# Performance work log

Measured on AMD Instinct MI355X. Metric: run time of the kernel, lower is better.

## Reference

```python
import jax, jax.numpy as jnp
import numpy as np

HID, AA, ESM = 128, 21, 320
D1 = HID + AA + ESM          # 469
N_GRAPHS = 64
BN_EPS = 1e-5


def _lin_params(key, din, dout):
    k1, k2 = jax.random.split(key)
    s = 1.0 / np.sqrt(din)
    W = jax.random.uniform(k1, (din, dout), jnp.float32, -s, s)
    b = jax.random.uniform(k2, (dout,), jnp.float32, -s, s)
    return W, b


def setup_inputs() -> dict:
    key = jax.random.key(0)
    ks = jax.random.split(key, 16)
    N, E = 30000, 480000
    inp = {
        'prot_x': jax.random.normal(ks[0], (N, 6485), jnp.float32),
        'prot_edge_index': jax.random.randint(ks[1], (2, E), 0, N, jnp.int64),
        'prot_batch': jnp.sort(jax.random.randint(ks[2], (N,), 0, N_GRAPHS, jnp.int64)),
    }
    inp['fl1_W'], inp['fl1_b'] = _lin_params(ks[3], 6165 - 21, HID)
    inp['fl2_W'], inp['fl2_b'] = _lin_params(ks[4], AA, AA)
    inp['fl3_W'], inp['fl3_b'] = _lin_params(ks[5], ESM, ESM)
    inp['pdb1_W'], inp['pdb1_b'] = _lin_params(ks[6], D1, D1)
    inp['pdb2_W'], inp['pdb2_b'] = _lin_params(ks[7], D1, 2 * D1)
    inp['af1_W'], inp['af1_b'] = _lin_params(ks[8], D1, D1)
    inp['af2_W'], inp['af2_b'] = _lin_params(ks[9], D1, 2 * D1)
    inp['pdb3_W'], inp['pdb3_b'] = _lin_params(ks[10], 4 * D1, 4 * D1)
    inp['fc1_W'], inp['fc1_b'] = _lin_params(ks[11], 4 * D1, 1024)
    inp['bn_g'] = jnp.ones((1024,), jnp.float32)
    inp['bn_b'] = jnp.zeros((1024,), jnp.float32)
    inp['fc2_W'], inp['fc2_b'] = _lin_params(ks[12], 1024, 486)
    return inp


def _gcn_graph(edge_index, n):
    # add self-loops, symmetric normalization D^-1/2 (A+I) D^-1/2
    loops = jnp.arange(n, dtype=edge_index.dtype)
    src = jnp.concatenate([edge_index[0], loops])
    dst = jnp.concatenate([edge_index[1], loops])
    deg = jax.ops.segment_sum(jnp.ones_like(dst, jnp.float32), dst, n)
    dinv = jax.lax.rsqrt(jnp.maximum(deg, 1.0))  # deg >= 1 via self-loop
    norm = dinv[src] * dinv[dst]
    return src, dst, norm


def _gcn_conv(x, W, b, src, dst, norm, n):
    h = x @ W                                   # [N, Dout]
    msg = h[src] * norm[:, None]                # gather + scale
    return jax.ops.segment_sum(msg, dst, n) + b  # scatter-add


def reference(prot_x, prot_edge_index, prot_batch,
              fl1_W, fl1_b, fl2_W, fl2_b, fl3_W, fl3_b,
              pdb1_W, pdb1_b, pdb2_W, pdb2_b,
              af1_W, af1_b, af2_W, af2_b,
              pdb3_W, pdb3_b, fc1_W, fc1_b, bn_g, bn_b, fc2_W, fc2_b):
    n = prot_x.shape[0]
    relu = jax.nn.relu
    f1 = relu(prot_x[:, 21:6165] @ fl1_W + fl1_b)   # [N,128]
    f2 = relu(prot_x[:, :21] @ fl2_W + fl2_b)       # [N,21]
    f3 = relu(prot_x[:, 6165:] @ fl3_W + fl3_b)     # [N,320]
    feat = jnp.concatenate([f2, f1, f3], axis=1)    # [N,469]

    src, dst, norm = _gcn_graph(prot_edge_index, n)
    x = relu(_gcn_conv(feat, pdb1_W, pdb1_b, src, dst, norm, n))
    x = relu(_gcn_conv(x, pdb2_W, pdb2_b, src, dst, norm, n))
    y = relu(_gcn_conv(feat, af1_W, af1_b, src, dst, norm, n))
    y = relu(_gcn_conv(y, af2_W, af2_b, src, dst, norm, n))
    z = jnp.concatenate([x, y], axis=1)             # [N, 4*469]
    z = relu(_gcn_conv(z, pdb3_W, pdb3_b, src, dst, norm, n))

    # gap: global mean pool per graph
    cnt = jax.ops.segment_sum(jnp.ones((n,), jnp.float32), prot_batch, N_GRAPHS)
    z = jax.ops.segment_sum(z, prot_batch, N_GRAPHS) / jnp.maximum(cnt, 1.0)[:, None]

    z = z @ fc1_W + fc1_b                            # [G,1024]
    mu = jnp.mean(z, axis=0)
    var = jnp.mean((z - mu) ** 2, axis=0)            # biased, torch BN training math
    z = (z - mu) * jax.lax.rsqrt(var + BN_EPS) * bn_g + bn_b
    z = relu(z)                                      # dropout = identity (eval)
    z = z @ fc2_W + fc2_b
    return jax.nn.sigmoid(z)
```

## Files before the change

### kernel.cpp

```cpp
#include <hip/hip_runtime.h>
#include <hip/hip_bf16.h>
#include <stdint.h>

#define NG 64

typedef __attribute__((ext_vector_type(8))) short bf16x8;
typedef __attribute__((ext_vector_type(4))) float f32x4;

#define AS1 __attribute__((address_space(1)))
#define AS3 __attribute__((address_space(3)))

static __device__ __forceinline__ unsigned short f2b(float f) {
    unsigned u = __float_as_uint(f);
    return (unsigned short)((u + 0x7fffu + ((u >> 16) & 1u)) >> 16);
}
static __device__ __forceinline__ float b2f(unsigned short h) {
    return __uint_as_float(((unsigned)h) << 16);
}
static __device__ __forceinline__ void gl16(const void* g, void* l) {
    __builtin_amdgcn_global_load_lds(
        (const AS1 void*)(uintptr_t)g,
        (AS3 void*)(unsigned)(uintptr_t)l, 16, 0, 0);
}

__global__ void initcnt_k(int* cnt, int n) {
    int i = blockIdx.x * blockDim.x + threadIdx.x;
    if (i < n) cnt[i] = 0;
}
__global__ void count_k(const int* __restrict__ dst, int* cnt, int E) {
    int e = blockIdx.x * blockDim.x + threadIdx.x;
    if (e < E) atomicAdd(&cnt[dst[e]], 1);
}
__global__ void dinv_k(const int* __restrict__ cnt, float* dinv, int n) {
    int i = blockIdx.x * blockDim.x + threadIdx.x;
    if (i < n) dinv[i] = rsqrtf((float)(cnt[i] + 1));
}
__global__ void exscan_k(const int* __restrict__ cnt, int* rowptr, int n) {
    __shared__ int wsum[16];
    __shared__ int carry;
    int tid = threadIdx.x, lane = tid & 63, wid = tid >> 6;
    if (tid == 0) { carry = 0; rowptr[0] = 0; }
    __syncthreads();
    for (int base = 0; base < n; base += 1024) {
        int i = base + tid;
        int x = (i < n) ? cnt[i] : 0;
#pragma unroll
        for (int off = 1; off < 64; off <<= 1) {
            int t = __shfl_up(x, off);
            if (lane >= off) x += t;
        }
        if (lane == 63) wsum[wid] = x;
        __syncthreads();
        if (tid < 16) {
            int s = wsum[tid];
#pragma unroll
            for (int off = 1; off < 16; off <<= 1) {
                int t = __shfl_up(s, off);
                if (tid >= off) s += t;
            }
            wsum[tid] = s;
        }
        __syncthreads();
        int add = carry + (wid ? wsum[wid - 1] : 0);
        if (i < n) rowptr[i + 1] = x + add;
        __syncthreads();
        if (tid == 1023) carry = x + add;
        __syncthreads();
    }
}
__global__ void fillinit_k(const int* __restrict__ rowptr, int* fill, int n) {
    int i = blockIdx.x * blockDim.x + threadIdx.x;
    if (i < n) fill[i] = rowptr[i];
}
__global__ void fill_k(const int* __restrict__ src, const int* __restrict__ dst,
                       int* fill, int* csr, int E) {
    int e = blockIdx.x * blockDim.x + threadIdx.x;
    if (e < E) {
        int d = dst[e];
        int pos = atomicAdd(&fill[d], 1);
        csr[pos] = src[e];
    }
}

__global__ void wtconv_k(const float* __restrict__ W, int K, int Nout,
                         unsigned short* __restrict__ Wt, int Kpad) {
    __shared__ float t[32][33];
    int k0 = blockIdx.x * 32, n0 = blockIdx.y * 32;
    int cx = threadIdx.x & 31, ry = threadIdx.x >> 5;
#pragma unroll
    for (int p = 0; p < 4; ++p) {
        int k = k0 + ry + p * 8, nn = n0 + cx;
        t[ry + p * 8][cx] = (k < K && nn < Nout) ? W[(size_t)k * Nout + nn] : 0.0f;
    }
    __syncthreads();
#pragma unroll
    for (int p = 0; p < 4; ++p) {
        int nn = n0 + ry + p * 8, k = k0 + cx;
        Wt[(size_t)nn * Kpad + k] = f2b(t[cx][ry + p * 8]);
    }
}

__global__ void fl2_k(const float* __restrict__ x, int ldx,
                      const float* __restrict__ W, const float* __restrict__ b,
                      unsigned short* __restrict__ out, int ldo, int n) {
    __shared__ float Ws[441];
    __shared__ float Bs[21];
    int tid = threadIdx.x;
    for (int i = tid; i < 441; i += 256) Ws[i] = W[i];
    if (tid < 21) Bs[tid] = b[tid];
    __syncthreads();
    int row = blockIdx.x * 256 + tid;
    if (row >= n) return;
    float xv[21];
#pragma unroll
    for (int j = 0; j < 21; ++j) xv[j] = x[(size_t)row * ldx + j];
    for (int c = 0; c < 21; ++c) {
        float a = Bs[c];
#pragma unroll
        for (int j = 0; j < 21; ++j) a = fmaf(xv[j], Ws[j * 21 + c], a);
        out[(size_t)row * ldo + c] = f2b(fmaxf(a, 0.0f));
    }
}

template<int BNT, bool A32>
__global__ __launch_bounds__(256) void mgemm_t(
    const void* __restrict__ Aptr, int lda, int Mreal,
    const unsigned short* __restrict__ Bt, int ldb,
    const float* __restrict__ bias,
    unsigned short* __restrict__ C, int ldc, int coff,
    int K, int Nout, int Nzero, int GX) {
    constexpr int NI = BNT / 32;
    __shared__ unsigned short As[128 * 32];
    __shared__ unsigned short Bs[BNT * 32];
    const int tid = threadIdx.x;
    const int w = tid >> 6, lane = tid & 63;

    const int nwg = gridDim.x;
    const int q = nwg >> 3, r = nwg & 7;
    const int xcd = blockIdx.x & 7, oidx = blockIdx.x >> 3;
    const int swz = (xcd < r ? xcd * (q + 1) : r * (q + 1) + (xcd - r) * q) + oidx;
    const int m0 = (swz / GX) * 128, n0 = (swz % GX) * BNT;

    const int wr = w >> 1, wc = w & 1;

    f32x4 acc[4][NI];
#pragma unroll
    for (int i = 0; i < 4; ++i)
#pragma unroll
        for (int j = 0; j < NI; ++j) acc[i][j] = (f32x4){0.f, 0.f, 0.f, 0.f};

    const int ko = (lane >> 4) * 8;
    const int rA = wr * 64 + (lane & 15);
    const int rB = wc * (BNT / 2) + (lane & 15);

    for (int k0 = 0; k0 < K; k0 += 32) {
        if constexpr (A32) {
            const float* Af = (const float*)Aptr;
#pragma unroll
            for (int j = 0; j < 2; ++j) {
                int c = w * 2 + j;
                int id2 = c * 64 + lane;
                int row = id2 >> 2, cc = id2 & 3;
                int gm = m0 + row; if (gm > Mreal - 1) gm = Mreal - 1;
                const float* ap = Af + (size_t)gm * lda + k0 + cc * 8;
                float4 v0 = *(const float4*)ap;
                float4 v1 = *(const float4*)(ap + 4);
                unsigned short t[8] = {f2b(v0.x), f2b(v0.y), f2b(v0.z), f2b(v0.w),
                                       f2b(v1.x), f2b(v1.y), f2b(v1.z), f2b(v1.w)};
                *(bf16x8*)&As[row * 32 + cc * 8] = *(const bf16x8*)t;
            }
        } else {
            const unsigned short* Ab = (const unsigned short*)Aptr;
#pragma unroll
            for (int j = 0; j < 2; ++j) {
                int c = w * 2 + j;
                int id2 = c * 64 + lane;
                int row = id2 >> 2, cc = id2 & 3;
                gl16(Ab + (size_t)(m0 + row) * lda + k0 + cc * 8, &As[c * 512]);
            }
        }
#pragma unroll
        for (int j = 0; j < BNT / 64; ++j) {
            int c = w * (BNT / 64) + j;
            int id2 = c * 64 + lane;
            int row = id2 >> 2, cc = id2 & 3;
            gl16(Bt + (size_t)(n0 + row) * ldb + k0 + cc * 8, &Bs[c * 512]);
        }
        __syncthreads();
        bf16x8 a[4], b[NI];
#pragma unroll
        for (int i = 0; i < 4; ++i) a[i] = *(const bf16x8*)&As[(rA + i * 16) * 32 + ko];
#pragma unroll
        for (int j = 0; j < NI; ++j) b[j] = *(const bf16x8*)&Bs[(rB + j * 16) * 32 + ko];
#pragma unroll
        for (int i = 0; i < 4; ++i)
#pragma unroll
            for (int j = 0; j < NI; ++j)
                acc[i][j] = __builtin_amdgcn_mfma_f32_16x16x32_bf16(a[i], b[j], acc[i][j], 0, 0, 0);
        __syncthreads();
    }

    const int cn = lane & 15, r4 = (lane >> 4) * 4;
    for (int ni = 0; ni < NI; ++ni) {
        int col = n0 + wc * (BNT / 2) + ni * 16 + cn;
        if (col >= Nzero) continue;
        bool real = col < Nout;
        float bb = real ? bias[col] : 0.0f;
#pragma unroll
        for (int mi = 0; mi < 4; ++mi) {
#pragma unroll
            for (int rr = 0; rr < 4; ++rr) {
                int row = m0 + wr * 64 + mi * 16 + r4 + rr;
                float x = real ? fmaxf(acc[mi][ni][rr] + bb, 0.0f) : 0.0f;
                C[(size_t)row * ldc + coff + col] = f2b(x);
            }
        }
    }
}

__global__ __launch_bounds__(256) void agg_wave_k(
    const unsigned short* __restrict__ in, unsigned short* __restrict__ out,
    const float* __restrict__ dinv, const int* __restrict__ rowptr,
    const int* __restrict__ csr, int D8, int ld, int n) {
    int lane = threadIdx.x & 63;
    int node = blockIdx.x * 4 + (threadIdx.x >> 6);
    if (node >= n) return;
    bool act = lane < D8;
    float di = dinv[node];
    float acc[8];
#pragma unroll
    for (int t = 0; t < 8; ++t) acc[t] = 0.0f;
    if (act) {
        bf16x8 v = *(const bf16x8*)(in + (size_t)node * ld + lane * 8);
#pragma unroll
        for (int t = 0; t < 8; ++t) acc[t] = di * b2f((unsigned short)v[t]);
    }
    int s = rowptr[node], e = rowptr[node + 1];
    for (int c = s; c < e; c += 64) {
        int m = e - c; if (m > 64) m = 64;
        int idx = (c + lane < e) ? csr[c + lane] : 0;
        float wl = dinv[idx];
        for (int j = 0; j < m; ++j) {
            int src = __shfl(idx, j);
            float wgt = __shfl(wl, j);
            if (act) {
                bf16x8 v = *(const bf16x8*)(in + (size_t)src * ld + lane * 8);
#pragma unroll
                for (int t = 0; t < 8; ++t) acc[t] = fmaf(wgt, b2f((unsigned short)v[t]), acc[t]);
            }
        }
    }
    if (act) {
        unsigned short o[8];
#pragma unroll
        for (int t = 0; t < 8; ++t) o[t] = f2b(di * acc[t]);
        *(bf16x8*)(out + (size_t)node * ld + lane * 8) = *(const bf16x8*)o;
    }
}

__global__ __launch_bounds__(256) void agg_block_k(
    const unsigned short* __restrict__ in, unsigned short* __restrict__ out,
    const float* __restrict__ dinv, const int* __restrict__ rowptr,
    const int* __restrict__ csr, int D8, int ld, int n) {
    int i = blockIdx.x;
    int tid = threadIdx.x;
    __shared__ int s_src[64];
    __shared__ float s_w[64];
    bool act = tid < D8;
    float di = dinv[i];
    float acc[8];
#pragma unroll
    for (int t = 0; t < 8; ++t) acc[t] = 0.0f;
    if (act) {
        bf16x8 v = *(const bf16x8*)(in + (size_t)i * ld + tid * 8);
#pragma unroll
        for (int t = 0; t < 8; ++t) acc[t] = di * b2f((unsigned short)v[t]);
    }
    int s = rowptr[i], e = rowptr[i + 1];
    for (int c = s; c < e; c += 64) {
        int k = c + tid;
        if (tid < 64 && k < e) { int sn = csr[k]; s_src[tid] = sn; s_w[tid] = dinv[sn]; }
        __syncthreads();
        int m = e - c; if (m > 64) m = 64;
        for (int j = 0; j < m; ++j) {
            int sn = s_src[j];
            float wgt = s_w[j];
            if (act) {
                bf16x8 v = *(const bf16x8*)(in + (size_t)sn * ld + tid * 8);
#pragma unroll
                for (int t = 0; t < 8; ++t) acc[t] = fmaf(wgt, b2f((unsigned short)v[t]), acc[t]);
            }
        }
        __syncthreads();
    }
    if (act) {
        unsigned short o[8];
#pragma unroll
        for (int t = 0; t < 8; ++t) o[t] = f2b(di * acc[t]);
        *(bf16x8*)(out + (size_t)i * ld + tid * 8) = *(const bf16x8*)o;
    }
}

__global__ void pool_k(const unsigned short* __restrict__ in, int ld,
                       const int* __restrict__ batch,
                       float* __restrict__ out, int n, int D) {
    int g = blockIdx.y;
    int d = blockIdx.x * blockDim.x + threadIdx.x;
    if (d >= D) return;
    int lo = 0, hi = n;
    while (lo < hi) { int mid = (lo + hi) >> 1; if (batch[mid] < g) lo = mid + 1; else hi = mid; }
    int start = lo;
    lo = start; hi = n;
    while (lo < hi) { int mid = (lo + hi) >> 1; if (batch[mid] < g + 1) lo = mid + 1; else hi = mid; }
    int end = lo;
    float sum = 0.0f;
    for (int r = start; r < end; r++) sum += b2f(in[(size_t)r * ld + d]);
    out[(size_t)g * D + d] = sum / fmaxf((float)(end - start), 1.0f);
}

__global__ __launch_bounds__(256) void sgemm_part_k(
    const float* __restrict__ A, int lda,
    const float* __restrict__ W, int ldw,
    float* __restrict__ part, int K, int Nout, int ksplit) {
    const int n0 = blockIdx.x * 64;
    const int ks = blockIdx.y;
    const int kbeg = (int)(((long long)K * ks) / ksplit);
    const int kend = (int)(((long long)K * (ks + 1)) / ksplit);
    const int tx = threadIdx.x & 63, ty = threadIdx.x >> 6;
    __shared__ float As[64][65];
    float acc[16];
#pragma unroll
    for (int r = 0; r < 16; ++r) acc[r] = 0.0f;

    for (int kb = kbeg; kb < kend; kb += 64) {
        int kc = kend - kb; if (kc > 64) kc = 64;
        for (int i = threadIdx.x; i < 64 * 64; i += 256) {
            int r = i >> 6, c = i & 63;
            As[r][c] = (c < kc) ? A[(size_t)r * lda + kb + c] : 0.0f;
        }
        __syncthreads();
        if (n0 + tx < Nout) {
            for (int k = 0; k < kc; ++k) {
                float w = W[(size_t)(kb + k) * ldw + n0 + tx];
#pragma unroll
                for (int r = 0; r < 16; ++r)
                    acc[r] = fmaf(As[ty * 16 + r][k], w, acc[r]);
            }
        }
        __syncthreads();
    }
    if (n0 + tx < Nout) {
#pragma unroll
        for (int r = 0; r < 16; ++r)
            part[((size_t)ks * 64 + ty * 16 + r) * Nout + n0 + tx] = acc[r];
    }
}

__global__ void sgemm_reduce_k(const float* __restrict__ part, const float* __restrict__ bias,
                               float* __restrict__ C, int ldc, int Nout, int ksplit, int act) {
    int i = blockIdx.x * blockDim.x + threadIdx.x;
    if (i >= NG * Nout) return;
    int m = i / Nout, n = i - m * Nout;
    float v = bias[n];
    for (int s = 0; s < ksplit; ++s) v += part[((size_t)s * 64 + m) * Nout + n];
    if (act == 2) v = 1.0f / (1.0f + expf(-v));
    C[(size_t)m * ldc + n] = v;
}

__global__ void bn_k(const float* __restrict__ z, const float* __restrict__ g,
                     const float* __restrict__ b, float* __restrict__ out) {
    int c = blockIdx.x * blockDim.x + threadIdx.x;
    if (c >= 1024) return;
    float s = 0.0f, s2 = 0.0f;
    for (int r = 0; r < NG; r++) { float v = z[r * 1024 + c]; s += v; s2 += v * v; }
    float mu = s / (float)NG;
    float var = s2 / (float)NG - mu * mu;
    float sc = g[c] * rsqrtf(var + 1e-5f);
    float sh = b[c] - mu * sc;
    for (int r = 0; r < NG; r++)
        out[r * 1024 + c] = fmaxf(fmaf(z[r * 1024 + c], sc, sh), 0.0f);
}

extern "C" void kernel_launch(void* const* d_in, const int* in_sizes, int n_in,
                              void* d_out, int out_size, void* d_ws, size_t ws_size,
                              hipStream_t stream) {
    (void)n_in; (void)out_size; (void)ws_size;
    const float* prot_x = (const float*)d_in[0];
    const int*   eidx   = (const int*)d_in[1];
    const int*   batch  = (const int*)d_in[2];
    const float* fl1_W = (const float*)d_in[3],  *fl1_b = (const float*)d_in[4];
    const float* fl2_W = (const float*)d_in[5],  *fl2_b = (const float*)d_in[6];
    const float* fl3_W = (const float*)d_in[7],  *fl3_b = (const float*)d_in[8];
    const float* pdb1_W = (const float*)d_in[9],  *pdb1_b = (const float*)d_in[10];
    const float* pdb2_W = (const float*)d_in[11], *pdb2_b = (const float*)d_in[12];
    const float* af1_W  = (const float*)d_in[13], *af1_b  = (const float*)d_in[14];
    const float* af2_W  = (const float*)d_in[15], *af2_b  = (const float*)d_in[16];
    const float* pdb3_W = (const float*)d_in[17], *pdb3_b = (const float*)d_in[18];
    const float* fc1_W  = (const float*)d_in[19], *fc1_b  = (const float*)d_in[20];
    const float* bn_g   = (const float*)d_in[21], *bn_b   = (const float*)d_in[22];
    const float* fc2_W  = (const float*)d_in[23], *fc2_b  = (const float*)d_in[24];

    const int N = in_sizes[2];
    const int E = in_sizes[1] / 2;
    const int* e_src = eidx;
    const int* e_dst = eidx + E;
    const int Mpad = ((N + 127) / 128) * 128;

    char* wp = (char*)d_ws;
    auto alloc = [&](size_t bytes) -> char* {
        char* r = wp; wp += (bytes + 255) & ~(size_t)255; return r;
    };
    unsigned short* feat = (unsigned short*)alloc((size_t)Mpad * 480 * 2);
    unsigned short* tmpb = (unsigned short*)alloc((size_t)Mpad * 480 * 2);
    unsigned short* hx   = (unsigned short*)alloc((size_t)Mpad * 480 * 2);
    unsigned short* hy   = (unsigned short*)alloc((size_t)Mpad * 480 * 2);
    unsigned short* zb   = (unsigned short*)alloc((size_t)Mpad * 1888 * 2);
    unsigned short* zagg = (unsigned short*)alloc((size_t)Mpad * 1888 * 2);
    unsigned short* wt_fl1  = (unsigned short*)alloc((size_t)128 * 6144 * 2);
    unsigned short* wt_fl3  = (unsigned short*)alloc((size_t)384 * 320 * 2);
    unsigned short* wt_pdb1 = (unsigned short*)alloc((size_t)512 * 480 * 2);
    unsigned short* wt_af1  = (unsigned short*)alloc((size_t)512 * 480 * 2);
    unsigned short* wt_pdb2 = (unsigned short*)alloc((size_t)1024 * 480 * 2);
    unsigned short* wt_af2  = (unsigned short*)alloc((size_t)1024 * 480 * 2);
    unsigned short* wt_pdb3 = (unsigned short*)alloc((size_t)1920 * 1888 * 2);
    float* f_dinv = (float*)alloc((size_t)N * 4);
    float* f_pool = (float*)alloc((size_t)NG * 1876 * 4);
    float* f_fc1  = (float*)alloc((size_t)NG * 1024 * 4);
    float* f_bn   = (float*)alloc((size_t)NG * 1024 * 4);
    float* f_part = (float*)alloc((size_t)16 * 64 * 1024 * 4);
    int* i_cnt    = (int*)alloc((size_t)N * 4);
    int* i_rowptr = (int*)alloc((size_t)(N + 1) * 4);
    int* i_fill   = (int*)alloc((size_t)N * 4);
    int* i_csr    = (int*)alloc((size_t)E * 4);

    auto mg128 = [&](const unsigned short* A, int lda, const unsigned short* Wt, int ldb,
                     const float* bias, unsigned short* C, int ldc, int coff,
                     int K, int Nout, int Nzero) {
        int gx = (Nzero + 127) / 128;
        mgemm_t<128, false><<<gx * (Mpad / 128), 256, 0, stream>>>(
            A, lda, Mpad, Wt, ldb, bias, C, ldc, coff, K, Nout, Nzero, gx);
    };
    auto mg64f = [&](const float* A, int lda, const unsigned short* Wt, int ldb,
                     const float* bias, unsigned short* C, int ldc, int coff,
                     int K, int Nout, int Nzero) {
        int gx = (Nzero + 63) / 64;
        mgemm_t<64, true><<<gx * (Mpad / 128), 256, 0, stream>>>(
            A, lda, N, Wt, ldb, bias, C, ldc, coff, K, Nout, Nzero, gx);
    };
    auto wt = [&](const float* W, int K, int Nout, unsigned short* Wt, int Kpad) {
        int Ntile = ((Nout + 127) / 128) * 128;
        wtconv_k<<<dim3(Kpad / 32, Ntile / 32), 256, 0, stream>>>(W, K, Nout, Wt, Kpad);
    };

    initcnt_k<<<(N + 255) / 256, 256, 0, stream>>>(i_cnt, N);
    count_k<<<(E + 255) / 256, 256, 0, stream>>>(e_dst, i_cnt, E);
    dinv_k<<<(N + 255) / 256, 256, 0, stream>>>(i_cnt, f_dinv, N);
    exscan_k<<<1, 1024, 0, stream>>>(i_cnt, i_rowptr, N);
    fillinit_k<<<(N + 255) / 256, 256, 0, stream>>>(i_rowptr, i_fill, N);
    fill_k<<<(E + 255) / 256, 256, 0, stream>>>(e_src, e_dst, i_fill, i_csr, E);

    wt(fl1_W, 6144, 128, wt_fl1, 6144);
    wt(fl3_W, 320, 320, wt_fl3, 320);
    wt(pdb1_W, 469, 469, wt_pdb1, 480);
    wt(af1_W, 469, 469, wt_af1, 480);
    wt(pdb2_W, 469, 938, wt_pdb2, 480);
    wt(af2_W, 469, 938, wt_af2, 480);
    wt(pdb3_W, 1876, 1876, wt_pdb3, 1888);

    fl2_k<<<(N + 255) / 256, 256, 0, stream>>>(prot_x, 6485, fl2_W, fl2_b, feat, 480, N);
    mg64f(prot_x + 21,   6485, wt_fl1, 6144, fl1_b, feat, 480, 21,  6144, 128, 128);
    mg64f(prot_x + 6165, 6485, wt_fl3, 320,  fl3_b, feat, 480, 149, 320,  320, 331);

    agg_wave_k<<<(N + 3) / 4, 256, 0, stream>>>(feat, tmpb, f_dinv, i_rowptr, i_csr, 60, 480, N);
    mg128(tmpb, 480, wt_pdb1, 480, pdb1_b, hx, 480, 0, 480, 469, 480);
    mg128(tmpb, 480, wt_af1, 480, af1_b, hy, 480, 0, 480, 469, 480);
    agg_wave_k<<<(N + 3) / 4, 256, 0, stream>>>(hx, tmpb, f_dinv, i_rowptr, i_csr, 60, 480, N);
    mg128(tmpb, 480, wt_pdb2, 480, pdb2_b, zb, 1888, 0, 480, 938, 938);
    agg_wave_k<<<(N + 3) / 4, 256, 0, stream>>>(hy, tmpb, f_dinv, i_rowptr, i_csr, 60, 480, N);
    mg128(tmpb, 480, wt_af2, 480, af2_b, zb, 1888, 938, 480, 938, 950);
    agg_block_k<<<N, 256, 0, stream>>>(zb, zagg, f_dinv, i_rowptr, i_csr, 236, 1888, N);
    mg128(zagg, 1888, wt_pdb3, 1888, pdb3_b, zb, 1888, 0, 1888, 1876, 1888);

    pool_k<<<dim3((1876 + 255) / 256, NG), 256, 0, stream>>>(zb, 1888, batch, f_pool, N, 1876);
    sgemm_part_k<<<dim3(16, 16), 256, 0, stream>>>(f_pool, 1876, fc1_W, 1024, f_part, 1876, 1024, 16);
    sgemm_reduce_k<<<(NG * 1024 + 255) / 256, 256, 0, stream>>>(f_part, fc1_b, f_fc1, 1024, 1024, 16, 0);
    bn_k<<<4, 256, 0, stream>>>(f_fc1, bn_g, bn_b, f_bn);
    sgemm_part_k<<<dim3(8, 16), 256, 0, stream>>>(f_bn, 1024, fc2_W, 486, f_part, 1024, 486, 16);
    sgemm_reduce_k<<<(NG * 486 + 255) / 256, 256, 0, stream>>>(f_part, fc2_b, (float*)d_out, 486, 486, 16, 2);
}
```

Baseline: 1.801 ms.

## Fuse paired GCN layer GEMMs and aggregations into wider concatenated passes

The pdb1 and af1 weights are concatenated into one 960-wide weight so a single GEMM produces both branches, and the two following 480-wide aggregations become one 960-wide aggregation pass over the CSR. The GEMM template drops the 64-wide N tile variant and always uses 128x128 tiles, including for the fp32-input feature GEMMs. Buffers are padded to 1920 columns and the final output goes to a separate buffer. This halves the number of edge-gather passes for layer two and the GEMM launches for layer one, at the cost of a larger padded K for the last GEMM and a different tile shape for the fl1/fl3 GEMMs.

```diff
diff --git a/kernel.cpp b/kernel.cpp
--- a/kernel.cpp
+++ b/kernel.cpp
@@ -83,7 +83,7 @@
 }
 
 __global__ void wtconv_k(const float* __restrict__ W, int K, int Nout,
-                         unsigned short* __restrict__ Wt, int Kpad) {
+                         unsigned short* __restrict__ Wt, int Kpad, int Nrows) {
     __shared__ float t[32][33];
     int k0 = blockIdx.x * 32, n0 = blockIdx.y * 32;
     int cx = threadIdx.x & 31, ry = threadIdx.x >> 5;
@@ -96,8 +96,17 @@
 #pragma unroll
     for (int p = 0; p < 4; ++p) {
         int nn = n0 + ry + p * 8, k = k0 + cx;
-        Wt[(size_t)nn * Kpad + k] = f2b(t[cx][ry + p * 8]);
-    }
+        if (nn < Nrows) Wt[(size_t)nn * Kpad + k] = f2b(t[cx][ry + p * 8]);
+    }
+}
+
+__global__ void biascat_k(const float* __restrict__ b0, const float* __restrict__ b1,
+                          float* __restrict__ out) {
+    int i = threadIdx.x + blockIdx.x * blockDim.x;
+    if (i >= 960) return;
+    int seg = i >= 480, c = i - seg * 480;
+    const float* b = seg ? b1 : b0;
+    out[i] = (c < 469) ? b[c] : 0.0f;
 }
 
 __global__ void fl2_k(const float* __restrict__ x, int ldx,
@@ -122,16 +131,15 @@
     }
 }
 
-template<int BNT, bool A32>
+template<bool A32>
 __global__ __launch_bounds__(256) void mgemm_t(
     const void* __restrict__ Aptr, int lda, int Mreal,
     const unsigned short* __restrict__ Bt, int ldb,
     const float* __restrict__ bias,
     unsigned short* __restrict__ C, int ldc, int coff,
     int K, int Nout, int Nzero, int GX) {
-    constexpr int NI = BNT / 32;
     __shared__ unsigned short As[128 * 32];
-    __shared__ unsigned short Bs[BNT * 32];
+    __shared__ unsigned short Bs[128 * 32];
     const int tid = threadIdx.x;
     const int w = tid >> 6, lane = tid & 63;
 
@@ -139,19 +147,19 @@
     const int q = nwg >> 3, r = nwg & 7;
     const int xcd = blockIdx.x & 7, oidx = blockIdx.x >> 3;
     const int swz = (xcd < r ? xcd * (q + 1) : r * (q + 1) + (xcd - r) * q) + oidx;
-    const int m0 = (swz / GX) * 128, n0 = (swz % GX) * BNT;
+    const int m0 = (swz / GX) * 128, n0 = (swz % GX) * 128;
 
     const int wr = w >> 1, wc = w & 1;
 
-    f32x4 acc[4][NI];
+    f32x4 acc[4][4];
 #pragma unroll
     for (int i = 0; i < 4; ++i)
 #pragma unroll
-        for (int j = 0; j < NI; ++j) acc[i][j] = (f32x4){0.f, 0.f, 0.f, 0.f};
+        for (int j = 0; j < 4; ++j) acc[i][j] = (f32x4){0.f, 0.f, 0.f, 0.f};
 
     const int ko = (lane >> 4) * 8;
     const int rA = wr * 64 + (lane & 15);
-    const int rB = wc * (BNT / 2) + (lane & 15);
+    const int rB = wc * 64 + (lane & 15);
 
     for (int k0 = 0; k0 < K; k0 += 32) {
         if constexpr (A32) {
@@ -180,29 +188,29 @@
             }
         }
 #pragma unroll
-        for (int j = 0; j < BNT / 64; ++j) {
-            int c = w * (BNT / 64) + j;
+        for (int j = 0; j < 2; ++j) {
+            int c = w * 2 + j;
             int id2 = c * 64 + lane;
             int row = id2 >> 2, cc = id2 & 3;
             gl16(Bt + (size_t)(n0 + row) * ldb + k0 + cc * 8, &Bs[c * 512]);
         }
         __syncthreads();
-        bf16x8 a[4], b[NI];
+        bf16x8 a[4], b[4];
 #pragma unroll
         for (int i = 0; i < 4; ++i) a[i] = *(const bf16x8*)&As[(rA + i * 16) * 32 + ko];
 #pragma unroll
-        for (int j = 0; j < NI; ++j) b[j] = *(const bf16x8*)&Bs[(rB + j * 16) * 32 + ko];
+        for (int j = 0; j < 4; ++j) b[j] = *(const bf16x8*)&Bs[(rB + j * 16) * 32 + ko];
 #pragma unroll
         for (int i = 0; i < 4; ++i)
 #pragma unroll
-            for (int j = 0; j < NI; ++j)
+            for (int j = 0; j < 4; ++j)
                 acc[i][j] = __builtin_amdgcn_mfma_f32_16x16x32_bf16(a[i], b[j], acc[i][j], 0, 0, 0);
         __syncthreads();
     }
 
     const int cn = lane & 15, r4 = (lane >> 4) * 4;
-    for (int ni = 0; ni < NI; ++ni) {
-        int col = n0 + wc * (BNT / 2) + ni * 16 + cn;
+    for (int ni = 0; ni < 4; ++ni) {
+        int col = n0 + wc * 64 + ni * 16 + cn;
         if (col >= Nzero) continue;
         bool real = col < Nout;
         float bb = real ? bias[col] : 0.0f;
@@ -258,7 +266,7 @@
     }
 }
 
-__global__ __launch_bounds__(256) void agg_block_k(
+__global__ void agg_block_k(
     const unsigned short* __restrict__ in, unsigned short* __restrict__ out,
     const float* __restrict__ dinv, const int* __restrict__ rowptr,
     const int* __restrict__ csr, int D8, int ld, int n) {
@@ -405,24 +413,26 @@
     const int* e_src = eidx;
     const int* e_dst = eidx + E;
     const int Mpad = ((N + 127) / 128) * 128;
+    const int MT = Mpad / 128;
 
     char* wp = (char*)d_ws;
     auto alloc = [&](size_t bytes) -> char* {
         char* r = wp; wp += (bytes + 255) & ~(size_t)255; return r;
     };
     unsigned short* feat = (unsigned short*)alloc((size_t)Mpad * 480 * 2);
-    unsigned short* tmpb = (unsigned short*)alloc((size_t)Mpad * 480 * 2);
-    unsigned short* hx   = (unsigned short*)alloc((size_t)Mpad * 480 * 2);
-    unsigned short* hy   = (unsigned short*)alloc((size_t)Mpad * 480 * 2);
-    unsigned short* zb   = (unsigned short*)alloc((size_t)Mpad * 1888 * 2);
-    unsigned short* zagg = (unsigned short*)alloc((size_t)Mpad * 1888 * 2);
+    unsigned short* tmp1 = (unsigned short*)alloc((size_t)Mpad * 480 * 2);
+    unsigned short* hxy  = (unsigned short*)alloc((size_t)Mpad * 960 * 2);
+    unsigned short* tmp2 = (unsigned short*)alloc((size_t)Mpad * 960 * 2);
+    unsigned short* zb   = (unsigned short*)alloc((size_t)Mpad * 1920 * 2);
+    unsigned short* zagg = (unsigned short*)alloc((size_t)Mpad * 1920 * 2);
+    unsigned short* zout = (unsigned short*)alloc((size_t)Mpad * 1888 * 2);
     unsigned short* wt_fl1  = (unsigned short*)alloc((size_t)128 * 6144 * 2);
     unsigned short* wt_fl3  = (unsigned short*)alloc((size_t)384 * 320 * 2);
-    unsigned short* wt_pdb1 = (unsigned short*)alloc((size_t)512 * 480 * 2);
-    unsigned short* wt_af1  = (unsigned short*)alloc((size_t)512 * 480 * 2);
+    unsigned short* wt_c1   = (unsigned short*)alloc((size_t)1024 * 480 * 2);
     unsigned short* wt_pdb2 = (unsigned short*)alloc((size_t)1024 * 480 * 2);
     unsigned short* wt_af2  = (unsigned short*)alloc((size_t)1024 * 480 * 2);
-    unsigned short* wt_pdb3 = (unsigned short*)alloc((size_t)1920 * 1888 * 2);
+    unsigned short* wt_pdb3 = (unsigned short*)alloc((size_t)1920 * 1920 * 2);
+    float* f_bias1 = (float*)alloc(960 * 4);
     float* f_dinv = (float*)alloc((size_t)N * 4);
     float* f_pool = (float*)alloc((size_t)NG * 1876 * 4);
     float* f_fc1  = (float*)alloc((size_t)NG * 1024 * 4);
@@ -433,23 +443,22 @@
     int* i_fill   = (int*)alloc((size_t)N * 4);
     int* i_csr    = (int*)alloc((size_t)E * 4);
 
-    auto mg128 = [&](const unsigned short* A, int lda, const unsigned short* Wt, int ldb,
-                     const float* bias, unsigned short* C, int ldc, int coff,
-                     int K, int Nout, int Nzero) {
+    auto mg = [&](const unsigned short* A, int lda, const unsigned short* Wt, int ldb,
+                  const float* bias, unsigned short* C, int ldc, int coff,
+                  int K, int Nout, int Nzero) {
         int gx = (Nzero + 127) / 128;
-        mgemm_t<128, false><<<gx * (Mpad / 128), 256, 0, stream>>>(
+        mgemm_t<false><<<gx * MT, 256, 0, stream>>>(
             A, lda, Mpad, Wt, ldb, bias, C, ldc, coff, K, Nout, Nzero, gx);
     };
-    auto mg64f = [&](const float* A, int lda, const unsigned short* Wt, int ldb,
-                     const float* bias, unsigned short* C, int ldc, int coff,
-                     int K, int Nout, int Nzero) {
-        int gx = (Nzero + 63) / 64;
-        mgemm_t<64, true><<<gx * (Mpad / 128), 256, 0, stream>>>(
+    auto mgf = [&](const float* A, int lda, const unsigned short* Wt, int ldb,
+                   const float* bias, unsigned short* C, int ldc, int coff,
+                   int K, int Nout, int Nzero) {
+        int gx = (Nzero + 127) / 128;
+        mgemm_t<true><<<gx * MT, 256, 0, stream>>>(
             A, lda, N, Wt, ldb, bias, C, ldc, coff, K, Nout, Nzero, gx);
     };
-    auto wt = [&](const float* W, int K, int Nout, unsigned short* Wt, int Kpad) {
-        int Ntile = ((Nout + 127) / 128) * 128;
-        wtconv_k<<<dim3(Kpad / 32, Ntile / 32), 256, 0, stream>>>(W, K, Nout, Wt, Kpad);
+    auto wt = [&](const float* W, int K, int Nout, unsigned short* Wt, int Kpad, int Nrows) {
+        wtconv_k<<<dim3(Kpad / 32, Nrows / 32), 256, 0, stream>>>(W, K, Nout, Wt, Kpad, Nrows);
     };
 
     initcnt_k<<<(N + 255) / 256, 256, 0, stream>>>(i_cnt, N);
@@ -459,29 +468,28 @@
     fillinit_k<<<(N + 255) / 256, 256, 0, stream>>>(i_rowptr, i_fill, N);
     fill_k<<<(E + 255) / 256, 256, 0, stream>>>(e_src, e_dst, i_fill, i_csr, E);
 
-    wt(fl1_W, 6144, 128, wt_fl1, 6144);
-    wt(fl3_W, 320, 320, wt_fl3, 320);
-    wt(pdb1_W, 469, 469, wt_pdb1, 480);
-    wt(af1_W, 469, 469, wt_af1, 480);
-    wt(pdb2_W, 469, 938, wt_pdb2, 480);
-    wt(af2_W, 469, 938, wt_af2, 480);
-    wt(pdb3_W, 1876, 1876, wt_pdb3, 1888);
+    wt(fl1_W, 6144, 128, wt_fl1, 6144, 128);
+    wt(fl3_W, 320, 320, wt_fl3, 320, 384);
+    wt(pdb1_W, 469, 469, wt_c1, 480, 480);
+    wt(af1_W, 469, 469, wt_c1 + (size_t)480 * 480, 480, 544);
+    wt(pdb2_W, 469, 938, wt_pdb2, 480, 1024);
+    wt(af2_W, 469, 938, wt_af2, 480, 1024);
+    wt(pdb3_W, 1876, 1876, wt_pdb3, 1920, 1920);
+    biascat_k<<<4, 256, 0, stream>>>(pdb1_b, af1_b, f_bias1);
 
     fl2_k<<<(N + 255) / 256, 256, 0, stream>>>(prot_x, 6485, fl2_W, fl2_b, feat, 480, N);
-    mg64f(prot_x + 21,   6485, wt_fl1, 6144, fl1_b, feat, 480, 21,  6144, 128, 128);
-    mg64f(prot_x + 6165, 6485, wt_fl3, 320,  fl3_b, feat, 480, 149, 320,  320, 331);
-
-    agg_wave_k<<<(N + 3) / 4, 256, 0, stream>>>(feat, tmpb, f_dinv, i_rowptr, i_csr, 60, 480, N);
-    mg128(tmpb, 480, wt_pdb1, 480, pdb1_b, hx, 480, 0, 480, 469, 480);
-    mg128(tmpb, 480, wt_af1, 480, af1_b, hy, 480, 0, 480, 469, 480);
-    agg_wave_k<<<(N + 3) / 4, 256, 0, stream>>>(hx, tmpb, f_dinv, i_rowptr, i_csr, 60, 480, N);
-    mg128(tmpb, 480, wt_pdb2, 480, pdb2_b, zb, 1888, 0, 480, 938, 938);
-    agg_wave_k<<<(N + 3) / 4, 256, 0, stream>>>(hy, tmpb, f_dinv, i_rowptr, i_csr, 60, 480, N);
-    mg128(tmpb, 480, wt_af2, 480, af2_b, zb, 1888, 938, 480, 938, 950);
-    agg_block_k<<<N, 256, 0, stream>>>(zb, zagg, f_dinv, i_rowptr, i_csr, 236, 1888, N);
-    mg128(zagg, 1888, wt_pdb3, 1888, pdb3_b, zb, 1888, 0, 1888, 1876, 1888);
-
-    pool_k<<<dim3((1876 + 255) / 256, NG), 256, 0, stream>>>(zb, 1888, batch, f_pool, N, 1876);
+    mgf(prot_x + 21,   6485, wt_fl1, 6144, fl1_b, feat, 480, 21,  6144, 128, 128);
+    mgf(prot_x + 6165, 6485, wt_fl3, 320,  fl3_b, feat, 480, 149, 320,  320, 331);
+
+    agg_wave_k<<<(N + 3) / 4, 256, 0, stream>>>(feat, tmp1, f_dinv, i_rowptr, i_csr, 60, 480, N);
+    mg(tmp1, 480, wt_c1, 480, f_bias1, hxy, 960, 0, 480, 960, 960);
+    agg_block_k<<<N, 128, 0, stream>>>(hxy, tmp2, f_dinv, i_rowptr, i_csr, 120, 960, N);
+    mg(tmp2,       960, wt_pdb2, 480, pdb2_b, zb, 1920, 0,   480, 938, 938);
+    mg(tmp2 + 480, 960, wt_af2,  480, af2_b,  zb, 1920, 938, 480, 938, 982);
+    agg_block_k<<<N, 256, 0, stream>>>(zb, zagg, f_dinv, i_rowptr, i_csr, 240, 1920, N);
+    mg(zagg, 1920, wt_pdb3, 1920, pdb3_b, zout, 1888, 0, 1920, 1876, 1876);
+
+    pool_k<<<dim3((1876 + 255) / 256, NG), 256, 0, stream>>>(zout, 1888, batch, f_pool, N, 1876);
     sgemm_part_k<<<dim3(16, 16), 256, 0, stream>>>(f_pool, 1876, fc1_W, 1024, f_part, 1876, 1024, 16);
     sgemm_reduce_k<<<(NG * 1024 + 255) / 256, 256, 0, stream>>>(f_part, fc1_b, f_fc1, 1024, 1024, 16, 0);
     bn_k<<<4, 256, 0, stream>>>(f_fc1, bn_g, bn_b, f_bn);
```

Result: faster. 1.742 ms (-3.3%).
